# Kernel tuning notes

Measured on AMD Instinct MI355X. Metric: run time of the kernel, lower is better.

## Reference

```python
import jax, jax.numpy as jnp
import numpy as np

N, E, G = 50000, 800000, 64
IN_NODE, OUT_NODE, IN_EDGE = 16, 20, 16
HID_E, N_ACT, HID_C = 64, 8, 256
BN_EPS = 1e-5


def setup_inputs() -> dict:
    key = jax.random.key(0)
    ks = jax.random.split(key, 12)
    def w(i, shape, scale=0.05):
        return jax.random.normal(ks[i], shape, jnp.float32) * scale
    return {
        "x": jax.random.normal(ks[0], (N, IN_NODE), jnp.float32),
        "edge_attr": jax.random.normal(ks[1], (E, IN_EDGE), jnp.float32),
        "a": jax.random.normal(ks[2], (G, N_ACT), jnp.float32),
        "edge_index": jax.random.randint(ks[3], (2, E), 0, N),
        "batch": jnp.sort(jax.random.randint(ks[4], (N,), 0, G)),
        # edge-conditioning MLP: Lin(16,64) -> BN(64) -> ReLU -> Lin(64, 16*20)
        "W1": w(5, (IN_EDGE, HID_E)), "b1": jnp.zeros((HID_E,), jnp.float32),
        "gamma": jnp.ones((HID_E,), jnp.float32), "beta": jnp.zeros((HID_E,), jnp.float32),
        "W2": w(6, (HID_E, IN_NODE * OUT_NODE)), "b2": jnp.zeros((IN_NODE * OUT_NODE,), jnp.float32),
        # NNConv root weight + bias
        "root_w": w(7, (IN_NODE, OUT_NODE)), "bias": jnp.zeros((OUT_NODE,), jnp.float32),
        # critic head: Lin(20+8,256) -> ReLU -> Lin(256,1)
        "Wc1": w(8, (OUT_NODE + N_ACT, HID_C)), "bc1": jnp.zeros((HID_C,), jnp.float32),
        "Wc2": w(9, (HID_C, 1)), "bc2": jnp.zeros((1,), jnp.float32),
    }


def reference(x, edge_attr, a, W1, b1, gamma, beta, W2, b2, root_w, bias,
              Wc1, bc1, Wc2, bc2, edge_index, batch):
    # edge-conditioning MLP (BatchNorm in training mode: batch stats over edges)
    h = edge_attr @ W1 + b1                              # [E, 64]
    mu = jnp.mean(h, axis=0)
    var = jnp.mean(jnp.square(h - mu), axis=0)           # biased var, as BN fwd
    h = (h - mu) * jax.lax.rsqrt(var + BN_EPS) * gamma + beta
    h = jax.nn.relu(h)
    w_e = (h @ W2 + b2).reshape(E, IN_NODE, OUT_NODE)    # per-edge weight matrix

    src, dst = edge_index[0], edge_index[1]
    msg = jnp.einsum('ei,eio->eo', x[src], w_e)          # gather + per-edge matvec [E, 20]
    aggr = jax.ops.segment_sum(msg, dst, num_segments=N) # scatter-add (NNConv aggr='add')
    out = x @ root_w + aggr + bias                       # [N, 20]

    # global mean pool over graphs
    sums = jax.ops.segment_sum(out, batch, num_segments=G)            # [G, 20]
    cnt = jax.ops.segment_sum(jnp.ones((N, 1), out.dtype), batch, num_segments=G)
    pooled = sums / jnp.maximum(cnt, 1.0)

    z = jnp.concatenate([pooled, a], axis=1)             # [G, 28]
    z = jax.nn.relu(z @ Wc1 + bc1)
    return z @ Wc2 + bc2                                 # [G, 1]
```

## Files before the change

### kernel.cpp

```cpp
#include <hip/hip_runtime.h>


#define E_EDGES   800000
#define N_NODES   50000
#define G_GRAPHS  64
#define EDGE_GRID 6144
#define NGROUPS   50000
#define GSTRIDE   1536
#define NSUP      256
#define STAT_GRID 512
#define QSCALE    131072.0f
#define QINV      (1.0f / 131072.0f)

typedef _Float16 f16x2 __attribute__((ext_vector_type(2)));
typedef _Float16 f16x8 __attribute__((ext_vector_type(8)));
typedef __fp16   fp16x2 __attribute__((ext_vector_type(2)));
typedef float    f32x4 __attribute__((ext_vector_type(4)));
typedef unsigned u32x4 __attribute__((ext_vector_type(4)));

union H2U { f16x2 h; unsigned u; };
union F8U { f16x8 v; f16x2 h2[4]; u32x4 u4; };

__device__ __forceinline__ f16x2 pkrtz(float a, float b) {
  fp16x2 r = __builtin_amdgcn_cvt_pkrtz(a, b);
  return __builtin_bit_cast(f16x2, r);
}

__device__ __forceinline__ int q17(float x) {
  float r = __builtin_fmaf(x, QSCALE, 12582912.0f);
  return __builtin_bit_cast(int, r) - 0x4B400000;
}

__global__ __launch_bounds__(256) void setup_kernel(
    const float* __restrict__ W2, const float* __restrict__ b2,
    const float* __restrict__ W1, const float* __restrict__ x,
    const float* __restrict__ ea, unsigned* __restrict__ Bbuf,
    unsigned* __restrict__ Bw1, unsigned* __restrict__ xh,
    float* __restrict__ gstatsT)
{
  __shared__ float red[4][272];
  const int b = blockIdx.x, tid = threadIdx.x;
  if (b < STAT_GRID) {
    int lane = tid & 63, wave = tid >> 6;
    int nl = lane & 15, q = lane >> 4;
    int gw = b * 4 + wave;
    f32x4 acc = (f32x4){0.f, 0.f, 0.f, 0.f};
    float ms = 0.f;
    for (int c0 = gw; c0 < E_EDGES / 32; c0 += STAT_GRID * 4) {
      const float* p = ea + (size_t)(c0 * 32 + q * 8) * 16 + nl;
      float v0 = p[0],  v1 = p[16], v2 = p[32], v3 = p[48];
      float v4 = p[64], v5 = p[80], v6 = p[96], v7 = p[112];
      ms += (v0 + v1) + (v2 + v3) + (v4 + v5) + (v6 + v7);
      F8U av;
      av.h2[0] = pkrtz(v0, v1); av.h2[1] = pkrtz(v2, v3);
      av.h2[2] = pkrtz(v4, v5); av.h2[3] = pkrtz(v6, v7);
      acc = __builtin_amdgcn_mfma_f32_16x16x32_f16(av.v, av.v, acc, 0, 0, 0);
    }
    ms += __shfl_xor(ms, 16, 64);
    ms += __shfl_xor(ms, 32, 64);
#pragma unroll
    for (int r = 0; r < 4; ++r) red[wave][(q * 4 + r) * 16 + nl] = acc[r];
    if (q == 0) red[wave][256 + nl] = ms;
    __syncthreads();
    for (int v = tid; v < 272; v += 256)
      gstatsT[(size_t)v * STAT_GRID + b] =
          red[0][v] + red[1][v] + red[2][v] + red[3][v];
  } else if (b < STAT_GRID + 70) {
    int idx = (b - STAT_GRID) * 256 + tid;
    if (idx < 33 * 512) {
      int r = idx & 3, lane = (idx >> 2) & 63, nt = (idx >> 8) & 1,
          s = idx >> 9;
      int q = lane >> 4, nl = lane & 15, n = nt * 16 + nl;
      float v0 = 0.f, v1 = 0.f;
      if (n < 20) {
        if (s < 32) {
          int K0 = s * 32 + q * 8 + 2 * r;
          v0 = W2[(K0 >> 4) * 320 + (K0 & 15) * 20 + n];
          v1 = W2[((K0 + 1) >> 4) * 320 + ((K0 + 1) & 15) * 20 + n];
        } else if (q < 2) {
          int i0 = q * 8 + 2 * r;
          v0 = b2[i0 * 20 + n];
          v1 = b2[(i0 + 1) * 20 + n];
        }
      }
      H2U pk; pk.h = pkrtz(v0, v1);
      Bbuf[idx] = pk.u;
    } else {
      int idx2 = idx - 33 * 512;
      int r = idx2 & 3, lane = (idx2 >> 2) & 63, nt = idx2 >> 8;
      int q = lane >> 4, nl = lane & 15, n = nt * 16 + nl;
      int k0 = q * 8 + 2 * r;
      float v0 = (k0 < 16)     ? W1[k0 * 64 + n]       : 0.f;
      float v1 = (k0 + 1 < 16) ? W1[(k0 + 1) * 64 + n] : 0.f;
      H2U pk; pk.h = pkrtz(v0, v1);
      Bw1[idx2] = pk.u;
    }
  } else {
    int i = (b - STAT_GRID - 70) * 256 + tid;
    if (i < N_NODES * 8) {
      H2U pk; pk.h = pkrtz(x[2 * i], x[2 * i + 1]);
      xh[i] = pk.u;
    }
  }
}

__global__ __launch_bounds__(256) void mid_kernel(
    const float* __restrict__ gstatsT, const float* __restrict__ W1,
    const float* __restrict__ b1, const float* __restrict__ gamma,
    const float* __restrict__ beta, const float* __restrict__ x,
    const int* __restrict__ batch, float* __restrict__ sc,
    float* __restrict__ sh, float* __restrict__ sumx,
    float* __restrict__ cntf)
{
  const int t = threadIdx.x;
  if (blockIdx.x == G_GRAPHS) {
    __shared__ float S[272];
    for (int v = t; v < 272; v += 256) {
      const float* p = gstatsT + (size_t)v * STAT_GRID;
      float s0 = 0.f, s1 = 0.f, s2 = 0.f, s3 = 0.f;
      for (int bb = 0; bb < STAT_GRID; bb += 4) {
        s0 += p[bb]; s1 += p[bb + 1]; s2 += p[bb + 2]; s3 += p[bb + 3];
      }
      S[v] = (s0 + s1) + (s2 + s3);
    }
    __syncthreads();
    if (t < 64) {
      float w[16];
#pragma unroll
      for (int j = 0; j < 16; ++j) w[j] = W1[j * 64 + t];
      const float invE = 1.0f / (float)E_EDGES;
      float mw = 0.f;
#pragma unroll
      for (int j = 0; j < 16; ++j) mw += S[256 + j] * w[j];
      mw *= invE;
      float qf = 0.f;
      for (int j = 0; j < 16; ++j) {
        float tt = 0.f;
#pragma unroll
        for (int j2 = 0; j2 < 16; ++j2) tt += S[j * 16 + j2] * w[j2];
        qf += w[j] * tt;
      }
      qf *= invE;
      float b = b1[t];
      float meanH = mw + b;
      float eh2 = qf + 2.f * b * mw + b * b;
      float var = eh2 - meanH * meanH;
      float s = gamma[t] * rsqrtf(var + 1e-5f);
      sc[t] = s;
      sh[t] = beta[t] + (b - meanH) * s;
    }
  } else {
    int g = blockIdx.x;
    __shared__ int se[2];
    if (t < 2) {
      int key = g + t;
      int lo = 0, hi = N_NODES;
      while (lo < hi) {
        int mid = (lo + hi) >> 1;
        if (batch[mid] < key) lo = mid + 1; else hi = mid;
      }
      se[t] = lo;
    }
    __syncthreads();
    int start = se[0], end = se[1];
    int c = t & 15, rr = t >> 4;
    float s = 0.f;
    for (int n = start + rr; n < end; n += 16) s += x[(size_t)n * 16 + c];
    __shared__ float red[256];
    red[t] = s;
    __syncthreads();
#pragma unroll
    for (int st = 128; st >= 16; st >>= 1) {
      if (t < st) red[t] += red[t + st];
      __syncthreads();
    }
    if (t < 16) sumx[g * 16 + t] = red[t];
    if (t == 0) cntf[g] = (float)(end - start);
  }
}

__global__ __launch_bounds__(64, 3) void edge_kernel(
    const unsigned* __restrict__ xh, const float* __restrict__ ea,
    const int* __restrict__ ei, const int* __restrict__ batch,
    const float* __restrict__ sc, const float* __restrict__ sh,
    const unsigned* __restrict__ Bbuf, const unsigned* __restrict__ Bw1v,
    int* __restrict__ gpartI)
{
  __shared__ unsigned hh[640];
  __shared__ int gacc[1280];
  const int lane = threadIdx.x;
  const int nl = lane & 15, q = lane >> 4;
  const int s = blockIdx.x;
  const int kq = (s >> 3) & 3;
  const int sgroup = ((s >> 5) << 3) | (s & 7);
  const int* srcp = ei;
  const int* dstp = ei + E_EDGES;

  for (int v = lane; v < 1280; v += 64) gacc[v] = 0;

  F8U bb[8][2];
#pragma unroll
  for (int sl = 0; sl < 8; ++sl)
#pragma unroll
    for (int nt = 0; nt < 2; ++nt)
      bb[sl][nt].u4 =
          ((const u32x4*)Bbuf)[((kq * 8 + sl) * 2 + nt) * 64 + lane];
  F8U bx[2];
  if (kq == 3) {
    bx[0].u4 = ((const u32x4*)Bbuf)[64 * 64 + lane];
    bx[1].u4 = ((const u32x4*)Bbuf)[65 * 64 + lane];
  } else {
    bx[0].u4 = (u32x4){0u, 0u, 0u, 0u};
    bx[1].u4 = (u32x4){0u, 0u, 0u, 0u};
  }
  F8U bw1; bw1.u4 = ((const u32x4*)Bw1v)[kq * 64 + lane];
  const float scv = sc[kq * 16 + nl];
  const float shv = sh[kq * 16 + nl];
  const int hrb = (q >> 1) * 20 + nl;
  const int qh = q & 1;

  int g = sgroup;
  f32x4 eaAn = (f32x4){0.f,0.f,0.f,0.f}, eaBn = eaAn;
  f32x4 eaA2 = eaAn, eaB2 = eaAn;
  u32x4 xp = (u32x4){0u,0u,0u,0u}, xpn = xp, xp2 = xp;
  int ge = 0, gen = 0, ge2 = 0;
  {
    int base = g * 16;
    if (q < 2) {
      const float* p = ea + (size_t)(base + nl) * 16 + q * 8;
      eaAn = *(const f32x4*)p;
      eaBn = *(const f32x4*)(p + 4);
    }
    int src = srcp[base + nl];
    xp = ((const u32x4*)xh)[src * 2 + qh];
    ge = batch[dstp[base + nl]];
  }
  {
    F8U aEA;
    if (q < 2) {
      aEA.h2[0] = pkrtz(eaAn[0], eaAn[1]); aEA.h2[1] = pkrtz(eaAn[2], eaAn[3]);
      aEA.h2[2] = pkrtz(eaBn[0], eaBn[1]); aEA.h2[3] = pkrtz(eaBn[2], eaBn[3]);
    } else {
      aEA.u4 = (u32x4){0u, 0u, 0u, 0u};
    }
    f32x4 hD = __builtin_amdgcn_mfma_f32_16x16x32_f16(
        aEA.v, bw1.v, (f32x4){0.f, 0.f, 0.f, 0.f}, 0, 0, 0);
#pragma unroll
    for (int r = 0; r < 4; ++r) {
      float h = fmaxf(hD[r] * scv + shv, 0.f);
      H2U pk; pk.h = pkrtz(h, h);
      hh[nl * 20 + q * 4 + r] = pk.u;
    }
  }
  if (g + GSTRIDE < NGROUPS) {
    int base = (g + GSTRIDE) * 16;
    if (q < 2) {
      const float* p = ea + (size_t)(base + nl) * 16 + q * 8;
      eaAn = *(const f32x4*)p;
      eaBn = *(const f32x4*)(p + 4);
    }
    int src = srcp[base + nl];
    xpn = ((const u32x4*)xh)[src * 2 + qh];
    gen = batch[dstp[base + nl]];
  }
  int cur = 0;

  while (g < NGROUPS) {
    const int gn = g + GSTRIDE, gnn = gn + GSTRIDE;
    const int hb = cur * 320 + hrb;

    unsigned hu[8];
#pragma unroll
    for (int sl = 0; sl < 8; ++sl) hu[sl] = hh[hb + sl * 40];
    const int gq0 = __shfl(ge, q * 4 + 0, 64);
    const int gq1 = __shfl(ge, q * 4 + 1, 64);
    const int gq2 = __shfl(ge, q * 4 + 2, 64);
    const int gq3 = __shfl(ge, q * 4 + 3, 64);

    f32x4 hDn = (f32x4){0.f, 0.f, 0.f, 0.f};
    const bool hvalid = (gn < NGROUPS);
    if (hvalid) {
      F8U aEA;
      if (q < 2) {
        aEA.h2[0] = pkrtz(eaAn[0], eaAn[1]);
        aEA.h2[1] = pkrtz(eaAn[2], eaAn[3]);
        aEA.h2[2] = pkrtz(eaBn[0], eaBn[1]);
        aEA.h2[3] = pkrtz(eaBn[2], eaBn[3]);
      } else {
        aEA.u4 = (u32x4){0u, 0u, 0u, 0u};
      }
      hDn = __builtin_amdgcn_mfma_f32_16x16x32_f16(
          aEA.v, bw1.v, (f32x4){0.f, 0.f, 0.f, 0.f}, 0, 0, 0);
    }

    if (gnn < NGROUPS) {
      int base = gnn * 16;
      if (q < 2) {
        const float* p = ea + (size_t)(base + nl) * 16 + q * 8;
        eaA2 = *(const f32x4*)p;
        eaB2 = *(const f32x4*)(p + 4);
      }
      int src = srcp[base + nl];
      xp2 = ((const u32x4*)xh)[src * 2 + qh];
      ge2 = batch[dstp[base + nl]];
    }

    F8U xcur; xcur.u4 = xp;
    f32x4 a00 = (f32x4){0.f, 0.f, 0.f, 0.f};
    f32x4 a01 = a00, a10 = a00, a11 = a00;
#pragma unroll
    for (int sl = 0; sl < 8; sl += 2) {
      H2U u0; u0.u = hu[sl];
      H2U u1; u1.u = hu[sl + 1];
      F8U av0, av1;
      av0.h2[0] = u0.h * xcur.h2[0];
      av0.h2[1] = u0.h * xcur.h2[1];
      av0.h2[2] = u0.h * xcur.h2[2];
      av0.h2[3] = u0.h * xcur.h2[3];
      av1.h2[0] = u1.h * xcur.h2[0];
      av1.h2[1] = u1.h * xcur.h2[1];
      av1.h2[2] = u1.h * xcur.h2[2];
      av1.h2[3] = u1.h * xcur.h2[3];
      a00 = __builtin_amdgcn_mfma_f32_16x16x32_f16(av0.v, bb[sl][0].v, a00,
                                                   0, 0, 0);
      a10 = __builtin_amdgcn_mfma_f32_16x16x32_f16(av0.v, bb[sl][1].v, a10,
                                                   0, 0, 0);
      a01 = __builtin_amdgcn_mfma_f32_16x16x32_f16(av1.v, bb[sl + 1][0].v,
                                                   a01, 0, 0, 0);
      a11 = __builtin_amdgcn_mfma_f32_16x16x32_f16(av1.v, bb[sl + 1][1].v,
                                                   a11, 0, 0, 0);
    }
    if (kq == 3) {
      F8U av;
      if (q < 2) av = xcur;
      else       av.u4 = (u32x4){0u, 0u, 0u, 0u};
      a00 = __builtin_amdgcn_mfma_f32_16x16x32_f16(av.v, bx[0].v, a00,
                                                   0, 0, 0);
      a10 = __builtin_amdgcn_mfma_f32_16x16x32_f16(av.v, bx[1].v, a10,
                                                   0, 0, 0);
    }
    const f32x4 acc0 = a00 + a01;
    const f32x4 acc1 = a10 + a11;

    if (hvalid) {
      const int hw = (cur ^ 1) * 320 + nl * 20 + q * 4;
#pragma unroll
      for (int r = 0; r < 4; ++r) {
        float h = fmaxf(hDn[r] * scv + shv, 0.f);
        H2U pk; pk.h = pkrtz(h, h);
        hh[hw + r] = pk.u;
      }
    }

    {
      int gi;
      gi = gq0 * 20;
      atomicAdd(&gacc[gi + nl], q17(acc0[0]));
      if (nl < 4) atomicAdd(&gacc[gi + 16 + nl], q17(acc1[0]));
      gi = gq1 * 20;
      atomicAdd(&gacc[gi + nl], q17(acc0[1]));
      if (nl < 4) atomicAdd(&gacc[gi + 16 + nl], q17(acc1[1]));
      gi = gq2 * 20;
      atomicAdd(&gacc[gi + nl], q17(acc0[2]));
      if (nl < 4) atomicAdd(&gacc[gi + 16 + nl], q17(acc1[2]));
      gi = gq3 * 20;
      atomicAdd(&gacc[gi + nl], q17(acc0[3]));
      if (nl < 4) atomicAdd(&gacc[gi + 16 + nl], q17(acc1[3]));
    }

    g = gn; cur ^= 1;
    xp = xpn; ge = gen;
    xpn = xp2; gen = ge2;
    eaAn = eaA2; eaBn = eaB2;
  }

  const int ssup = s & (NSUP - 1);
  for (int v = lane; v < 1280; v += 64) {
    int gg = v / 20, o = v - gg * 20;
    atomicAdd(&gpartI[(gg * NSUP + ssup) * 20 + o], gacc[v]);
  }
}

__global__ __launch_bounds__(256) void critic_kernel(
    const int* __restrict__ gpartI, const float* __restrict__ sumx,
    const float* __restrict__ cntf, const float* __restrict__ root_w,
    const float* __restrict__ bias, const float* __restrict__ a,
    const float* __restrict__ Wc1, const float* __restrict__ bc1,
    const float* __restrict__ Wc2, const float* __restrict__ bc2,
    float* __restrict__ out)
{
  int g = blockIdx.x, t = threadIdx.x;
  __shared__ int part[240];
  __shared__ float pooled[20];
  if (t < 240) {
    int col = t % 20, r = t / 20;
    int s = 0;
    const int* gp = gpartI + (size_t)g * NSUP * 20;
    for (int sl = r; sl < NSUP; sl += 12) s += gp[sl * 20 + col];
    part[t] = s;
  }
  __syncthreads();
  if (t < 20) {
    int si = 0;
#pragma unroll
    for (int r = 0; r < 12; ++r) si += part[r * 20 + t];
    float s = (float)si * QINV;
    float cnt = cntf[g];
    float base = bias[t] * cnt;
#pragma unroll
    for (int i = 0; i < 16; ++i) base += sumx[g * 16 + i] * root_w[i * 20 + t];
    pooled[t] = (s + base) / fmaxf(cnt, 1.f);
  }
  __syncthreads();
  float z = bc1[t];
#pragma unroll
  for (int j = 0; j < 20; ++j) z += pooled[j] * Wc1[j * 256 + t];
#pragma unroll
  for (int j = 0; j < 8; ++j) z += a[g * 8 + j] * Wc1[(20 + j) * 256 + t];
  z = fmaxf(z, 0.f);
  float pr = z * Wc2[t];
#pragma unroll
  for (int off = 32; off >= 1; off >>= 1) pr += __shfl_down(pr, off, 64);
  __shared__ float red[4];
  if ((t & 63) == 0) red[t >> 6] = pr;
  __syncthreads();
  if (t == 0) out[g] = red[0] + red[1] + red[2] + red[3] + bc2[0];
}

extern "C" void kernel_launch(void* const* d_in, const int* in_sizes, int n_in,
                              void* d_out, int out_size, void* d_ws,
                              size_t ws_size, hipStream_t stream) {
  const float* x         = (const float*)d_in[0];
  const float* edge_attr = (const float*)d_in[1];
  const float* a         = (const float*)d_in[2];
  const int*   ei        = (const int*)d_in[3];
  const int*   batch     = (const int*)d_in[4];
  const float* W1        = (const float*)d_in[5];
  const float* b1        = (const float*)d_in[6];
  const float* gamma     = (const float*)d_in[7];
  const float* beta      = (const float*)d_in[8];
  const float* W2        = (const float*)d_in[9];
  const float* b2        = (const float*)d_in[10];
  const float* root_w    = (const float*)d_in[11];
  const float* bias      = (const float*)d_in[12];
  const float* Wc1       = (const float*)d_in[13];
  const float* bc1       = (const float*)d_in[14];
  const float* Wc2       = (const float*)d_in[15];
  const float* bc2       = (const float*)d_in[16];
  float* out = (float*)d_out;

  float* wsf     = (float*)d_ws;
  float* sc      = wsf;
  float* sh      = wsf + 64;
  float* sumx    = wsf + 128;
  float* cntf    = wsf + 1152;
  unsigned* Bw1  = (unsigned*)(wsf + 1216);
  unsigned* Bbuf = (unsigned*)(wsf + 2240);
  float* gstatsT = wsf + 19136;
  unsigned* xhp  = (unsigned*)(wsf + 158400);
  int* gpartI    = (int*)(wsf + 558400);

  (void)hipMemsetAsync(gpartI, 0, (size_t)G_GRAPHS * NSUP * 20 * sizeof(int),
                       stream);

  const int XCONV_BLOCKS = (N_NODES * 8 + 255) / 256;
  setup_kernel<<<STAT_GRID + 70 + XCONV_BLOCKS, 256, 0, stream>>>(
      W2, b2, W1, x, edge_attr, Bbuf, Bw1, xhp, gstatsT);
  mid_kernel<<<G_GRAPHS + 1, 256, 0, stream>>>(gstatsT, W1, b1, gamma, beta,
                                               x, batch, sc, sh, sumx, cntf);
  edge_kernel<<<EDGE_GRID, 64, 0, stream>>>(xhp, edge_attr, ei, batch, sc,
                                            sh, Bbuf, Bw1, gpartI);
  critic_kernel<<<G_GRAPHS, 256, 0, stream>>>(gpartI, sumx, cntf, root_w,
                                              bias, a, Wc1, bc1, Wc2, bc2,
                                              out);
}
```

Before: 239.5 us.

## Restructure edge-loop prefetch so dependent gathers issue one stage later; wave-reduce stats

```diff
diff --git a/kernel.cpp b/kernel.cpp
--- a/kernel.cpp
+++ b/kernel.cpp
@@ -115,13 +115,18 @@
   const int t = threadIdx.x;
   if (blockIdx.x == G_GRAPHS) {
     __shared__ float S[272];
-    for (int v = t; v < 272; v += 256) {
+    int wave = t >> 6, lane = t & 63;
+    for (int v = wave; v < 272; v += 4) {
       const float* p = gstatsT + (size_t)v * STAT_GRID;
-      float s0 = 0.f, s1 = 0.f, s2 = 0.f, s3 = 0.f;
-      for (int bb = 0; bb < STAT_GRID; bb += 4) {
-        s0 += p[bb]; s1 += p[bb + 1]; s2 += p[bb + 2]; s3 += p[bb + 3];
-      }
-      S[v] = (s0 + s1) + (s2 + s3);
+      float s = 0.f;
+      for (int bb = lane; bb < STAT_GRID; bb += 64) s += p[bb];
+      s += __shfl_xor(s, 32, 64);
+      s += __shfl_xor(s, 16, 64);
+      s += __shfl_xor(s, 8, 64);
+      s += __shfl_xor(s, 4, 64);
+      s += __shfl_xor(s, 2, 64);
+      s += __shfl_xor(s, 1, 64);
+      if (lane == 0) S[v] = s;
     }
     __syncthreads();
     if (t < 64) {
@@ -220,26 +225,31 @@
   const int qh = q & 1;
 
   int g = sgroup;
+  u32x4 xp  = (u32x4){0u,0u,0u,0u};
+  int   ge20 = 0;
   f32x4 eaAn = (f32x4){0.f,0.f,0.f,0.f}, eaBn = eaAn;
+  int   srcn = 0, dstn = 0;
   f32x4 eaA2 = eaAn, eaB2 = eaAn;
-  u32x4 xp = (u32x4){0u,0u,0u,0u}, xpn = xp, xp2 = xp;
-  int ge = 0, gen = 0, ge2 = 0;
+  int   src2 = 0, dst2 = 0;
+  u32x4 xpn = xp;
+  int   gen20 = 0;
+
   {
-    int base = g * 16;
+    int base = g * 16 + nl;
+    int src0 = srcp[base];
+    int dst0 = dstp[base];
+    xp = ((const u32x4*)xh)[src0 * 2 + qh];
+    ge20 = batch[dst0] * 20;
+    f32x4 eaA0 = (f32x4){0.f,0.f,0.f,0.f}, eaB0 = eaA0;
     if (q < 2) {
-      const float* p = ea + (size_t)(base + nl) * 16 + q * 8;
-      eaAn = *(const f32x4*)p;
-      eaBn = *(const f32x4*)(p + 4);
-    }
-    int src = srcp[base + nl];
-    xp = ((const u32x4*)xh)[src * 2 + qh];
-    ge = batch[dstp[base + nl]];
-  }
-  {
+      const float* p = ea + (size_t)base * 16 + q * 8;
+      eaA0 = *(const f32x4*)p;
+      eaB0 = *(const f32x4*)(p + 4);
+    }
     F8U aEA;
     if (q < 2) {
-      aEA.h2[0] = pkrtz(eaAn[0], eaAn[1]); aEA.h2[1] = pkrtz(eaAn[2], eaAn[3]);
-      aEA.h2[2] = pkrtz(eaBn[0], eaBn[1]); aEA.h2[3] = pkrtz(eaBn[2], eaBn[3]);
+      aEA.h2[0] = pkrtz(eaA0[0], eaA0[1]); aEA.h2[1] = pkrtz(eaA0[2], eaA0[3]);
+      aEA.h2[2] = pkrtz(eaB0[0], eaB0[1]); aEA.h2[3] = pkrtz(eaB0[2], eaB0[3]);
     } else {
       aEA.u4 = (u32x4){0u, 0u, 0u, 0u};
     }
@@ -253,32 +263,45 @@
     }
   }
   if (g + GSTRIDE < NGROUPS) {
-    int base = (g + GSTRIDE) * 16;
+    int base = (g + GSTRIDE) * 16 + nl;
+    srcn = srcp[base];
+    dstn = dstp[base];
     if (q < 2) {
-      const float* p = ea + (size_t)(base + nl) * 16 + q * 8;
+      const float* p = ea + (size_t)base * 16 + q * 8;
       eaAn = *(const f32x4*)p;
       eaBn = *(const f32x4*)(p + 4);
     }
-    int src = srcp[base + nl];
-    xpn = ((const u32x4*)xh)[src * 2 + qh];
-    gen = batch[dstp[base + nl]];
   }
   int cur = 0;
 
   while (g < NGROUPS) {
     const int gn = g + GSTRIDE, gnn = gn + GSTRIDE;
-    const int hb = cur * 320 + hrb;
+    const bool hvalid = (gn < NGROUPS);
+
+    if (gnn < NGROUPS) {
+      int base = gnn * 16 + nl;
+      src2 = srcp[base];
+      dst2 = dstp[base];
+      if (q < 2) {
+        const float* p = ea + (size_t)base * 16 + q * 8;
+        eaA2 = *(const f32x4*)p;
+        eaB2 = *(const f32x4*)(p + 4);
+      }
+    }
+    if (hvalid) {
+      xpn = ((const u32x4*)xh)[srcn * 2 + qh];
+      gen20 = batch[dstn] * 20;
+    }
 
     unsigned hu[8];
 #pragma unroll
-    for (int sl = 0; sl < 8; ++sl) hu[sl] = hh[hb + sl * 40];
-    const int gq0 = __shfl(ge, q * 4 + 0, 64);
-    const int gq1 = __shfl(ge, q * 4 + 1, 64);
-    const int gq2 = __shfl(ge, q * 4 + 2, 64);
-    const int gq3 = __shfl(ge, q * 4 + 3, 64);
+    for (int sl = 0; sl < 8; ++sl) hu[sl] = hh[cur * 320 + hrb + sl * 40];
+    const int gq0 = __shfl(ge20, q * 4 + 0, 64);
+    const int gq1 = __shfl(ge20, q * 4 + 1, 64);
+    const int gq2 = __shfl(ge20, q * 4 + 2, 64);
+    const int gq3 = __shfl(ge20, q * 4 + 3, 64);
 
     f32x4 hDn = (f32x4){0.f, 0.f, 0.f, 0.f};
-    const bool hvalid = (gn < NGROUPS);
     if (hvalid) {
       F8U aEA;
       if (q < 2) {
@@ -291,18 +314,6 @@
       }
       hDn = __builtin_amdgcn_mfma_f32_16x16x32_f16(
           aEA.v, bw1.v, (f32x4){0.f, 0.f, 0.f, 0.f}, 0, 0, 0);
-    }
-
-    if (gnn < NGROUPS) {
-      int base = gnn * 16;
-      if (q < 2) {
-        const float* p = ea + (size_t)(base + nl) * 16 + q * 8;
-        eaA2 = *(const f32x4*)p;
-        eaB2 = *(const f32x4*)(p + 4);
-      }
-      int src = srcp[base + nl];
-      xp2 = ((const u32x4*)xh)[src * 2 + qh];
-      ge2 = batch[dstp[base + nl]];
     }
 
     F8U xcur; xcur.u4 = xp;
@@ -353,24 +364,19 @@
     }
 
     {
-      int gi;
-      gi = gq0 * 20;
-      atomicAdd(&gacc[gi + nl], q17(acc0[0]));
-      if (nl < 4) atomicAdd(&gacc[gi + 16 + nl], q17(acc1[0]));
-      gi = gq1 * 20;
-      atomicAdd(&gacc[gi + nl], q17(acc0[1]));
-      if (nl < 4) atomicAdd(&gacc[gi + 16 + nl], q17(acc1[1]));
-      gi = gq2 * 20;
-      atomicAdd(&gacc[gi + nl], q17(acc0[2]));
-      if (nl < 4) atomicAdd(&gacc[gi + 16 + nl], q17(acc1[2]));
-      gi = gq3 * 20;
-      atomicAdd(&gacc[gi + nl], q17(acc0[3]));
-      if (nl < 4) atomicAdd(&gacc[gi + 16 + nl], q17(acc1[3]));
+      atomicAdd(&gacc[gq0 + nl], q17(acc0[0]));
+      if (nl < 4) atomicAdd(&gacc[gq0 + 16 + nl], q17(acc1[0]));
+      atomicAdd(&gacc[gq1 + nl], q17(acc0[1]));
+      if (nl < 4) atomicAdd(&gacc[gq1 + 16 + nl], q17(acc1[1]));
+      atomicAdd(&gacc[gq2 + nl], q17(acc0[2]));
+      if (nl < 4) atomicAdd(&gacc[gq2 + 16 + nl], q17(acc1[2]));
+      atomicAdd(&gacc[gq3 + nl], q17(acc0[3]));
+      if (nl < 4) atomicAdd(&gacc[gq3 + 16 + nl], q17(acc1[3]));
     }
 
     g = gn; cur ^= 1;
-    xp = xpn; ge = gen;
-    xpn = xp2; gen = ge2;
+    xp = xpn; ge20 = gen20;
+    srcn = src2; dstn = dst2;
     eaAn = eaA2; eaBn = eaB2;
   }
 
```

Result: slower. 386.3 us (+61.3%).
